# Optimization experiments

Hardware: AMD Instinct MI355X
Metric: run time of the kernel (lower is better)

## Reference

```python
import jax, jax.numpy as jnp
import numpy as np

HIDDEN = 1024
EMBED = HIDDEN // 4
SEQ = 512
BATCH = 256
NUM_CLASSES = 10


def setup_inputs() -> dict:
    key = jax.random.key(0)
    ks = jax.random.split(key, 16)

    def w(k, d1, d2):
        # kaiming_normal_ with nonlinearity='linear': std = 1/sqrt(fan_in=d2)
        return jax.random.normal(k, (d1, d2), dtype=jnp.float32) / jnp.sqrt(d2)

    inp = {
        "x": jax.random.randint(ks[0], (BATCH, SEQ), 0, 3),
        "emb": jax.random.normal(ks[1], (3, EMBED), dtype=jnp.float32),
        "w_gx": w(ks[2], EMBED, HIDDEN), "w_gh": w(ks[3], HIDDEN, HIDDEN), "b_g": jnp.zeros((HIDDEN,), jnp.float32),
        "w_ix": w(ks[4], EMBED, HIDDEN), "w_ih": w(ks[5], HIDDEN, HIDDEN), "b_i": jnp.zeros((HIDDEN,), jnp.float32),
        "w_fx": w(ks[6], EMBED, HIDDEN), "w_fh": w(ks[7], HIDDEN, HIDDEN), "b_f": jnp.zeros((HIDDEN,), jnp.float32),
        "w_ox": w(ks[8], EMBED, HIDDEN), "w_oh": w(ks[9], HIDDEN, HIDDEN), "b_o": jnp.zeros((HIDDEN,), jnp.float32),
        "w_ph": w(ks[10], HIDDEN, NUM_CLASSES), "b_p": jnp.zeros((NUM_CLASSES,), jnp.float32),
    }
    return inp


def reference(x, emb, w_gx, w_gh, b_g, w_ix, w_ih, b_i, w_fx, w_fh, b_f,
              w_ox, w_oh, b_o, w_ph, b_p):
    B, T = x.shape
    embedded = emb[x]                         # [B, T, E]
    pad = ((x + 1) // 2).astype(emb.dtype)    # [B, T]

    xs = (jnp.swapaxes(embedded, 0, 1),       # [T, B, E]
          jnp.swapaxes(pad, 0, 1))            # [T, B]

    h0 = jnp.zeros((B, w_gh.shape[0]), emb.dtype)
    c0 = jnp.zeros_like(h0)

    def step(carry, inputs):
        h, c = carry
        xt, pt = inputs
        g = jnp.tanh(xt @ w_gx + h @ w_gh + b_g)
        i = jax.nn.sigmoid(xt @ w_ix + h @ w_ih + b_i)
        f = jax.nn.sigmoid(xt @ w_fx + h @ w_fh + b_f)
        o = jax.nn.sigmoid(xt @ w_ox + h @ w_oh + b_o)
        c = g * i + c * f
        h = jnp.tanh(c) * o
        c = c * pt[:, None]
        return (h, c), None

    (h, _), _ = jax.lax.scan(step, (h0, c0), xs)
    p = h @ w_ph + b_p                        # [B, num_classes]
    # Faithful to original: log_softmax over dim=0 (batch dim)
    return jax.nn.log_softmax(p, axis=0)
```

## Files before the change

### kernel.cpp

```cpp
#include <hip/hip_runtime.h>
#include <hip/hip_bf16.h>

#define T_SEQ 512
#define BATCH 256
#define HID   1024
#define EMBD  256
#define NCLS  10

typedef __bf16 bf16x8 __attribute__((ext_vector_type(8)));
typedef float  floatx16 __attribute__((ext_vector_type(16)));
typedef float  floatx2 __attribute__((ext_vector_type(2)));
typedef unsigned short ushortx8 __attribute__((ext_vector_type(8)));

__device__ __forceinline__ unsigned int f2bf(float f) {
    unsigned int u = __builtin_bit_cast(unsigned int, f);
    u += 0x7fffu + ((u >> 16) & 1u);
    return u >> 16;
}
__device__ __forceinline__ float sig_fast(float x) {
    return __builtin_amdgcn_rcpf(1.0f + __expf(-x));
}
__device__ __forceinline__ float tanh_fast(float x) {
    return 1.0f - 2.0f * __builtin_amdgcn_rcpf(1.0f + __expf(2.0f * x));
}

__global__ void prep_xw_kernel(const float* __restrict__ emb,
                               const float* __restrict__ wgx, const float* __restrict__ wix,
                               const float* __restrict__ wfx, const float* __restrict__ wox,
                               const float* __restrict__ bg,  const float* __restrict__ bi,
                               const float* __restrict__ bf,  const float* __restrict__ bo,
                               float* __restrict__ XW) {
    int gid = blockIdx.x * blockDim.x + threadIdx.x;
    if (gid >= 3 * 4 * HID) return;
    int tok  = gid >> 12;
    int gate = (gid >> 10) & 3;
    int n    = gid & 1023;
    const float* W = gate == 0 ? wgx : gate == 1 ? wix : gate == 2 ? wfx : wox;
    const float* B = gate == 0 ? bg  : gate == 1 ? bi  : gate == 2 ? bf  : bo;
    float acc = B[n];
    const float* e = emb + tok * EMBD;
    for (int k = 0; k < EMBD; ++k) acc += e[k] * W[k * HID + n];
    XW[gid] = acc;
}

__global__ void prep_w_kernel(const float* __restrict__ wgh, const float* __restrict__ wih,
                              const float* __restrict__ wfh, const float* __restrict__ woh,
                              unsigned short* __restrict__ Wt) {
    int bid = blockIdx.x;
    int w   = bid & 31;
    int i   = (bid >> 5) & 31;
    int kh  = (bid >> 10) & 1;
    int g   = bid >> 11;
    const float* W = g == 0 ? wgh : g == 1 ? wih : g == 2 ? wfh : woh;
    int lane = threadIdx.x;
    int j    = w * 32 + (lane & 31);
    int k0   = kh * 512 + i * 16 + (lane >> 5) * 8;
    ushortx8 o8;
    #pragma unroll
    for (int e = 0; e < 8; ++e) o8[e] = (unsigned short)f2bf(W[(k0 + e) * HID + j]);
    int frag = ((w * 4 + g) * 2 + kh) * 32 + i;
    *(ushortx8*)&Wt[frag * 512 + lane * 8] = o8;
}

__global__ __launch_bounds__(512, 2)
void lstm_kernel(const int* __restrict__ x, const float* __restrict__ XW,
                 const unsigned short* __restrict__ Wt,
                 unsigned int* __restrict__ hbuf32, int* __restrict__ flags,
                 int* __restrict__ xflag) {
    __shared__ unsigned short hs[32 * 1032];
    __shared__ float gbuf[8 * 32 * 36];
    __shared__ float xwl[384];
    __shared__ unsigned char xtok[32 * 512];
    __shared__ int use_local_sh;

    const int tid  = threadIdx.x;
    const int grp  = blockIdx.x & 7;
    const int w    = blockIdx.x >> 3;
    const int wv   = tid >> 6;
    const int gv   = wv >> 1;
    const int kh   = wv & 1;
    const int lane = tid & 63;
    const int m32  = lane & 31;
    const int hv5  = lane >> 5;

    {
        int xcc = 0;
        asm volatile("s_getreg_b32 %0, hwreg(HW_REG_XCC_ID)" : "=s"(xcc));
        if (tid == 0) {
            __hip_atomic_store(&xflag[grp * 32 + w], xcc + 1, __ATOMIC_RELAXED,
                               __HIP_MEMORY_SCOPE_SYSTEM);
        }
        if (wv == 0) {
            int v;
            for (;;) {
                v = __hip_atomic_load(&xflag[grp * 32 + (lane & 31)], __ATOMIC_RELAXED,
                                      __HIP_MEMORY_SCOPE_SYSTEM);
                if (__all(v != 0)) break;
                __builtin_amdgcn_s_sleep(2);
            }
            int v0 = __shfl(v, 0, 64);
            if (lane == 0) use_local_sh = __all(v == v0) ? 1 : 0;
        }
    }

    bf16x8 Bf[32];
    {
        const unsigned short* wb = Wt + (size_t)(((w * 4 + gv) * 2 + kh) * 32) * 512
                                      + (size_t)lane * 8;
        #pragma unroll
        for (int i = 0; i < 32; ++i)
            Bf[i] = *(const bf16x8*)(wb + i * 512);
    }
    if (tid < 384) {
        int tok = tid >> 7, g = (tid >> 5) & 3, jl = tid & 31;
        xwl[tid] = XW[(tok * 4 + g) * HID + w * 32 + jl];
    }
    #pragma unroll
    for (int it = 0; it < 32; ++it) {
        int flat = it * 512 + tid;
        int row  = flat >> 9;
        int col  = flat & 511;
        xtok[flat] = (unsigned char)x[(grp * 32 + row) * T_SEQ + col];
    }
    __syncthreads();
    const bool use_local = (use_local_sh != 0);

    const int erow = tid >> 4;
    const int jc2  = tid & 15;
    float cst[2] = {0.f, 0.f};
    unsigned long long* hs64 = (unsigned long long*)hs;

    for (int s = 0; s < T_SEQ; ++s) {
        if (s > 0) {
            if (wv == 0) {
                const int fidx = grp * 32 + (lane & 31);
                if (use_local) {
                    while (__hip_atomic_load(&flags[fidx], __ATOMIC_RELAXED,
                                             __HIP_MEMORY_SCOPE_AGENT) < s)
                        __builtin_amdgcn_s_sleep(1);
                } else {
                    while (__hip_atomic_load(&flags[fidx], __ATOMIC_RELAXED,
                                             __HIP_MEMORY_SCOPE_SYSTEM) < s)
                        __builtin_amdgcn_s_sleep(1);
                }
            }
            __syncthreads();
        }

        const unsigned long long* hp64 = (const unsigned long long*)
            (hbuf32 + (size_t)(s & 1) * (BATCH * HID / 2)) + (size_t)grp * 32 * 256;
        {
            unsigned long long tmp[16];
            if (use_local) {
                #pragma unroll
                for (int it = 0; it < 16; ++it) {
                    int flat = it * 512 + tid;
                    tmp[it] = __hip_atomic_load(&hp64[(flat >> 8) * 256 + (flat & 255)],
                                                __ATOMIC_RELAXED, __HIP_MEMORY_SCOPE_AGENT);
                }
            } else {
                #pragma unroll
                for (int it = 0; it < 16; ++it) {
                    int flat = it * 512 + tid;
                    tmp[it] = __hip_atomic_load(&hp64[(flat >> 8) * 256 + (flat & 255)],
                                                __ATOMIC_RELAXED, __HIP_MEMORY_SCOPE_SYSTEM);
                }
            }
            #pragma unroll
            for (int it = 0; it < 16; ++it) {
                int flat = it * 512 + tid;
                hs64[(flat >> 8) * 258 + (flat & 255)] = tmp[it];
            }
        }
        __syncthreads();

        floatx16 acc = {0.f,0.f,0.f,0.f,0.f,0.f,0.f,0.f,0.f,0.f,0.f,0.f,0.f,0.f,0.f,0.f};
        const unsigned short* ap = hs + m32 * 1032 + kh * 512 + hv5 * 8;
        #pragma unroll
        for (int i = 0; i < 32; ++i) {
            bf16x8 a = *(const bf16x8*)(ap + i * 16);
            acc = __builtin_amdgcn_mfma_f32_32x32x16_bf16(a, Bf[i], acc, 0, 0, 0);
        }

        {
            float* gb = &gbuf[(size_t)(gv * 2 + kh) * 32 * 36];
            #pragma unroll
            for (int reg = 0; reg < 16; ++reg) {
                int row = (reg & 3) + 8 * (reg >> 2) + 4 * hv5;
                gb[row * 36 + m32] = acc[reg];
            }
        }
        __syncthreads();

        {
            int tk = xtok[erow * 512 + s];
            const float* xb = &xwl[tk * 128];
            const int go = erow * 36 + jc2 * 2;
            floatx2 ag = *(const floatx2*)&gbuf[0 * 32 * 36 + go]
                       + *(const floatx2*)&gbuf[1 * 32 * 36 + go];
            floatx2 ai = *(const floatx2*)&gbuf[2 * 32 * 36 + go]
                       + *(const floatx2*)&gbuf[3 * 32 * 36 + go];
            floatx2 af = *(const floatx2*)&gbuf[4 * 32 * 36 + go]
                       + *(const floatx2*)&gbuf[5 * 32 * 36 + go];
            floatx2 ao = *(const floatx2*)&gbuf[6 * 32 * 36 + go]
                       + *(const floatx2*)&gbuf[7 * 32 * 36 + go];
            floatx2 xg = *(const floatx2*)&xb[0 * 32 + jc2 * 2];
            floatx2 xi = *(const floatx2*)&xb[1 * 32 + jc2 * 2];
            floatx2 xf = *(const floatx2*)&xb[2 * 32 + jc2 * 2];
            floatx2 xo = *(const floatx2*)&xb[3 * 32 + jc2 * 2];
            unsigned int hvv[2];
            #pragma unroll
            for (int u = 0; u < 2; ++u) {
                float g  = tanh_fast(ag[u] + xg[u]);
                float ii = sig_fast(ai[u] + xi[u]);
                float ff = sig_fast(af[u] + xf[u]);
                float oo = sig_fast(ao[u] + xo[u]);
                float cn = g * ii + cst[u] * ff;
                float h  = tanh_fast(cn) * oo;
                cst[u]   = (tk != 0) ? cn : 0.0f;
                hvv[u]   = f2bf(h);
            }
            unsigned int* hnext = hbuf32 + (size_t)((s + 1) & 1) * (BATCH * HID / 2);
            unsigned int* hp = &hnext[((grp * 32 + erow) * HID + w * 32 + jc2 * 2) >> 1];
            unsigned int hval = hvv[0] | (hvv[1] << 16);
            if (use_local) {
                __hip_atomic_store(hp, hval, __ATOMIC_RELAXED, __HIP_MEMORY_SCOPE_WORKGROUP);
            } else {
                __hip_atomic_store(hp, hval, __ATOMIC_RELAXED, __HIP_MEMORY_SCOPE_SYSTEM);
            }
        }
        __syncthreads();

        if (s < T_SEQ - 1 && tid == 0) {
            if (use_local) {
                __hip_atomic_store(&flags[grp * 32 + w], s + 1,
                                   __ATOMIC_RELAXED, __HIP_MEMORY_SCOPE_WORKGROUP);
            } else {
                __hip_atomic_store(&flags[grp * 32 + w], s + 1,
                                   __ATOMIC_RELAXED, __HIP_MEMORY_SCOPE_SYSTEM);
            }
        }
    }
}

__global__ void proj_kernel(const unsigned short* __restrict__ h,
                            const float* __restrict__ wph, const float* __restrict__ bp,
                            float* __restrict__ out) {
    __shared__ float wl[HID * NCLS];
    __shared__ float red[256];
    int tid = threadIdx.x;
    for (int i = tid; i < HID * NCLS; i += 256) wl[i] = wph[i];
    __syncthreads();
    float p[NCLS];
    #pragma unroll
    for (int c2 = 0; c2 < NCLS; ++c2) p[c2] = bp[c2];
    const unsigned short* hr = h + tid * HID;
    for (int k0 = 0; k0 < HID / 8; ++k0) {
        bf16x8 hv = *(const bf16x8*)(hr + k0 * 8);
        #pragma unroll
        for (int j = 0; j < 8; ++j) {
            float hk = (float)hv[j];
            #pragma unroll
            for (int c2 = 0; c2 < NCLS; ++c2) p[c2] += hk * wl[(k0 * 8 + j) * NCLS + c2];
        }
    }
    for (int c2 = 0; c2 < NCLS; ++c2) {
        red[tid] = p[c2];
        __syncthreads();
        for (int s = 128; s > 0; s >>= 1) {
            if (tid < s) red[tid] = fmaxf(red[tid], red[tid + s]);
            __syncthreads();
        }
        float mx = red[0];
        __syncthreads();
        red[tid] = __expf(p[c2] - mx);
        __syncthreads();
        for (int s = 128; s > 0; s >>= 1) {
            if (tid < s) red[tid] += red[tid + s];
            __syncthreads();
        }
        float lse = mx + __logf(red[0]);
        __syncthreads();
        out[tid * NCLS + c2] = p[c2] - lse;
    }
}

extern "C" void kernel_launch(void* const* d_in, const int* in_sizes, int n_in,
                              void* d_out, int out_size, void* d_ws, size_t ws_size,
                              hipStream_t stream) {
    const int*   x    = (const int*)d_in[0];
    const float* emb  = (const float*)d_in[1];
    const float* wgx  = (const float*)d_in[2];
    const float* wgh  = (const float*)d_in[3];
    const float* bg_  = (const float*)d_in[4];
    const float* wix  = (const float*)d_in[5];
    const float* wih  = (const float*)d_in[6];
    const float* bi_  = (const float*)d_in[7];
    const float* wfx  = (const float*)d_in[8];
    const float* wfh  = (const float*)d_in[9];
    const float* bf_  = (const float*)d_in[10];
    const float* wox  = (const float*)d_in[11];
    const float* woh  = (const float*)d_in[12];
    const float* bo_  = (const float*)d_in[13];
    const float* wph  = (const float*)d_in[14];
    const float* bp_  = (const float*)d_in[15];
    float* out = (float*)d_out;

    char* wsp = (char*)d_ws;
    int*            flags = (int*)wsp;
    int*            xflag = (int*)(wsp + 4096);
    float*          XW    = (float*)(wsp + 8192);
    unsigned short* Wt    = (unsigned short*)(wsp + 8192 + 49152);
    unsigned int*   hbuf32= (unsigned int*)(wsp + 8192 + 49152 + 8388608);

    hipMemsetAsync(flags, 0, 8192, stream);
    hipMemsetAsync(hbuf32, 0, BATCH * HID * sizeof(unsigned short), stream);

    prep_xw_kernel<<<48, 256, 0, stream>>>(emb, wgx, wix, wfx, wox,
                                           bg_, bi_, bf_, bo_, XW);
    prep_w_kernel<<<8192, 64, 0, stream>>>(wgh, wih, wfh, woh, Wt);

    void* args[] = { (void*)&x, (void*)&XW, (void*)&Wt, (void*)&hbuf32,
                     (void*)&flags, (void*)&xflag };
    hipError_t cerr = hipLaunchCooperativeKernel((void*)lstm_kernel, dim3(256), dim3(512),
                                                 args, 0, stream);
    if (cerr != hipSuccess) {
        lstm_kernel<<<dim3(256), dim3(512), 0, stream>>>(x, XW, Wt, hbuf32, flags, xflag);
    }

    proj_kernel<<<1, 256, 0, stream>>>((const unsigned short*)hbuf32, wph, bp_, out);
}
```

Baseline: 1.777 ms.

## Read h directly from global into MFMA operands, split K four ways

```diff
diff --git a/kernel.cpp b/kernel.cpp
--- a/kernel.cpp
+++ b/kernel.cpp
@@ -46,19 +46,22 @@
 __global__ void prep_w_kernel(const float* __restrict__ wgh, const float* __restrict__ wih,
                               const float* __restrict__ wfh, const float* __restrict__ woh,
                               unsigned short* __restrict__ Wt) {
-    int bid = blockIdx.x;
-    int w   = bid & 31;
-    int i   = (bid >> 5) & 31;
-    int kh  = (bid >> 10) & 1;
-    int g   = bid >> 11;
+    int bid  = blockIdx.x;
+    int gsub = bid & 1;
+    int i    = (bid >> 1) & 15;
+    int kq   = (bid >> 5) & 3;
+    int gp   = (bid >> 7) & 1;
+    int w    = bid >> 8;
+    int g    = gp * 2 + gsub;
     const float* W = g == 0 ? wgh : g == 1 ? wih : g == 2 ? wfh : woh;
     int lane = threadIdx.x;
     int j    = w * 32 + (lane & 31);
-    int k0   = kh * 512 + i * 16 + (lane >> 5) * 8;
+    int kk   = kq * 16 + i;
+    int k0   = kk * 16 + (lane >> 5) * 8;
     ushortx8 o8;
     #pragma unroll
     for (int e = 0; e < 8; ++e) o8[e] = (unsigned short)f2bf(W[(k0 + e) * HID + j]);
-    int frag = ((w * 4 + g) * 2 + kh) * 32 + i;
+    int frag = (((w * 2 + gp) * 4 + kq) * 16 + i) * 2 + gsub;
     *(ushortx8*)&Wt[frag * 512 + lane * 8] = o8;
 }
 
@@ -67,8 +70,7 @@
                  const unsigned short* __restrict__ Wt,
                  unsigned int* __restrict__ hbuf32, int* __restrict__ flags,
                  int* __restrict__ xflag) {
-    __shared__ unsigned short hs[32 * 1032];
-    __shared__ float gbuf[8 * 32 * 36];
+    __shared__ float gbuf[16 * 32 * 36];
     __shared__ float xwl[384];
     __shared__ unsigned char xtok[32 * 512];
     __shared__ int use_local_sh;
@@ -77,8 +79,8 @@
     const int grp  = blockIdx.x & 7;
     const int w    = blockIdx.x >> 3;
     const int wv   = tid >> 6;
-    const int gv   = wv >> 1;
-    const int kh   = wv & 1;
+    const int gp   = wv >> 2;
+    const int kq   = wv & 3;
     const int lane = tid & 63;
     const int m32  = lane & 31;
     const int hv5  = lane >> 5;
@@ -105,11 +107,11 @@
 
     bf16x8 Bf[32];
     {
-        const unsigned short* wb = Wt + (size_t)(((w * 4 + gv) * 2 + kh) * 32) * 512
+        const unsigned short* wb = Wt + (size_t)(((w * 2 + gp) * 4 + kq) * 32) * 512
                                       + (size_t)lane * 8;
         #pragma unroll
-        for (int i = 0; i < 32; ++i)
-            Bf[i] = *(const bf16x8*)(wb + i * 512);
+        for (int t = 0; t < 32; ++t)
+            Bf[t] = *(const bf16x8*)(wb + t * 512);
     }
     if (tid < 384) {
         int tok = tid >> 7, g = (tid >> 5) & 3, jl = tid & 31;
@@ -128,7 +130,7 @@
     const int erow = tid >> 4;
     const int jc2  = tid & 15;
     float cst[2] = {0.f, 0.f};
-    unsigned long long* hs64 = (unsigned long long*)hs;
+    const unsigned short* hb = (const unsigned short*)hbuf32;
 
     for (int s = 0; s < T_SEQ; ++s) {
         if (s > 0) {
@@ -147,47 +149,38 @@
             __syncthreads();
         }
 
-        const unsigned long long* hp64 = (const unsigned long long*)
-            (hbuf32 + (size_t)(s & 1) * (BATCH * HID / 2)) + (size_t)grp * 32 * 256;
+        const unsigned short* hp = hb + (size_t)(s & 1) * (BATCH * HID)
+                                 + ((grp * 32 + m32) * HID + kq * 256 + hv5 * 8);
+        floatx16 acc0 = {0.f,0.f,0.f,0.f,0.f,0.f,0.f,0.f,0.f,0.f,0.f,0.f,0.f,0.f,0.f,0.f};
+        floatx16 acc1 = {0.f,0.f,0.f,0.f,0.f,0.f,0.f,0.f,0.f,0.f,0.f,0.f,0.f,0.f,0.f,0.f};
+        if (use_local) {
+            asm volatile("buffer_inv" ::: "memory");
+            #pragma unroll
+            for (int i = 0; i < 16; ++i) {
+                bf16x8 a = *(const bf16x8*)(hp + i * 16);
+                acc0 = __builtin_amdgcn_mfma_f32_32x32x16_bf16(a, Bf[2 * i],     acc0, 0, 0, 0);
+                acc1 = __builtin_amdgcn_mfma_f32_32x32x16_bf16(a, Bf[2 * i + 1], acc1, 0, 0, 0);
+            }
+        } else {
+            #pragma unroll
+            for (int i = 0; i < 16; ++i) {
+                union { unsigned long long q[2]; bf16x8 a; } u;
+                const unsigned long long* qp = (const unsigned long long*)(hp + i * 16);
+                u.q[0] = __hip_atomic_load(qp,     __ATOMIC_RELAXED, __HIP_MEMORY_SCOPE_SYSTEM);
+                u.q[1] = __hip_atomic_load(qp + 1, __ATOMIC_RELAXED, __HIP_MEMORY_SCOPE_SYSTEM);
+                acc0 = __builtin_amdgcn_mfma_f32_32x32x16_bf16(u.a, Bf[2 * i],     acc0, 0, 0, 0);
+                acc1 = __builtin_amdgcn_mfma_f32_32x32x16_bf16(u.a, Bf[2 * i + 1], acc1, 0, 0, 0);
+            }
+        }
+
         {
-            unsigned long long tmp[16];
-            if (use_local) {
-                #pragma unroll
-                for (int it = 0; it < 16; ++it) {
-                    int flat = it * 512 + tid;
-                    tmp[it] = __hip_atomic_load(&hp64[(flat >> 8) * 256 + (flat & 255)],
-                                                __ATOMIC_RELAXED, __HIP_MEMORY_SCOPE_AGENT);
-                }
-            } else {
-                #pragma unroll
-                for (int it = 0; it < 16; ++it) {
-                    int flat = it * 512 + tid;
-                    tmp[it] = __hip_atomic_load(&hp64[(flat >> 8) * 256 + (flat & 255)],
-                                                __ATOMIC_RELAXED, __HIP_MEMORY_SCOPE_SYSTEM);
-                }
-            }
-            #pragma unroll
-            for (int it = 0; it < 16; ++it) {
-                int flat = it * 512 + tid;
-                hs64[(flat >> 8) * 258 + (flat & 255)] = tmp[it];
-            }
-        }
-        __syncthreads();
-
-        floatx16 acc = {0.f,0.f,0.f,0.f,0.f,0.f,0.f,0.f,0.f,0.f,0.f,0.f,0.f,0.f,0.f,0.f};
-        const unsigned short* ap = hs + m32 * 1032 + kh * 512 + hv5 * 8;
-        #pragma unroll
-        for (int i = 0; i < 32; ++i) {
-            bf16x8 a = *(const bf16x8*)(ap + i * 16);
-            acc = __builtin_amdgcn_mfma_f32_32x32x16_bf16(a, Bf[i], acc, 0, 0, 0);
-        }
-
-        {
-            float* gb = &gbuf[(size_t)(gv * 2 + kh) * 32 * 36];
+            float* gb0 = &gbuf[(size_t)((gp * 2 + 0) * 4 + kq) * 1152];
+            float* gb1 = &gbuf[(size_t)((gp * 2 + 1) * 4 + kq) * 1152];
             #pragma unroll
             for (int reg = 0; reg < 16; ++reg) {
                 int row = (reg & 3) + 8 * (reg >> 2) + 4 * hv5;
-                gb[row * 36 + m32] = acc[reg];
+                gb0[row * 36 + m32] = acc0[reg];
+                gb1[row * 36 + m32] = acc1[reg];
             }
         }
         __syncthreads();
@@ -196,14 +189,15 @@
             int tk = xtok[erow * 512 + s];
             const float* xb = &xwl[tk * 128];
             const int go = erow * 36 + jc2 * 2;
-            floatx2 ag = *(const floatx2*)&gbuf[0 * 32 * 36 + go]
-                       + *(const floatx2*)&gbuf[1 * 32 * 36 + go];
-            floatx2 ai = *(const floatx2*)&gbuf[2 * 32 * 36 + go]
-                       + *(const floatx2*)&gbuf[3 * 32 * 36 + go];
-            floatx2 af = *(const floatx2*)&gbuf[4 * 32 * 36 + go]
-                       + *(const floatx2*)&gbuf[5 * 32 * 36 + go];
-            floatx2 ao = *(const floatx2*)&gbuf[6 * 32 * 36 + go]
-                       + *(const floatx2*)&gbuf[7 * 32 * 36 + go];
+            #define GSUM(g) ( *(const floatx2*)&gbuf[((g) * 4 + 0) * 1152 + go] \
+                            + *(const floatx2*)&gbuf[((g) * 4 + 1) * 1152 + go] \
+                            + *(const floatx2*)&gbuf[((g) * 4 + 2) * 1152 + go] \
+                            + *(const floatx2*)&gbuf[((g) * 4 + 3) * 1152 + go] )
+            floatx2 ag = GSUM(0);
+            floatx2 ai = GSUM(1);
+            floatx2 af = GSUM(2);
+            floatx2 ao = GSUM(3);
+            #undef GSUM
             floatx2 xg = *(const floatx2*)&xb[0 * 32 + jc2 * 2];
             floatx2 xi = *(const floatx2*)&xb[1 * 32 + jc2 * 2];
             floatx2 xf = *(const floatx2*)&xb[2 * 32 + jc2 * 2];
@@ -221,12 +215,12 @@
                 hvv[u]   = f2bf(h);
             }
             unsigned int* hnext = hbuf32 + (size_t)((s + 1) & 1) * (BATCH * HID / 2);
-            unsigned int* hp = &hnext[((grp * 32 + erow) * HID + w * 32 + jc2 * 2) >> 1];
+            unsigned int* hpst = &hnext[((grp * 32 + erow) * HID + w * 32 + jc2 * 2) >> 1];
             unsigned int hval = hvv[0] | (hvv[1] << 16);
             if (use_local) {
-                __hip_atomic_store(hp, hval, __ATOMIC_RELAXED, __HIP_MEMORY_SCOPE_WORKGROUP);
+                __hip_atomic_store(hpst, hval, __ATOMIC_RELAXED, __HIP_MEMORY_SCOPE_WORKGROUP);
             } else {
-                __hip_atomic_store(hp, hval, __ATOMIC_RELAXED, __HIP_MEMORY_SCOPE_SYSTEM);
+                __hip_atomic_store(hpst, hval, __ATOMIC_RELAXED, __HIP_MEMORY_SCOPE_SYSTEM);
             }
         }
         __syncthreads();
```

Result: slower. 2.643 ms (+48.7%).

## Split h-load into K halves with shared-memory counters instead of block barrier

Applied to the files above, without the earlier changes.

```diff
diff --git a/kernel.cpp b/kernel.cpp
--- a/kernel.cpp
+++ b/kernel.cpp
@@ -71,6 +71,7 @@
     __shared__ float gbuf[8 * 32 * 36];
     __shared__ float xwl[384];
     __shared__ unsigned char xtok[32 * 512];
+    __shared__ int scnt[2];
     __shared__ int use_local_sh;
 
     const int tid  = threadIdx.x;
@@ -115,6 +116,7 @@
         int tok = tid >> 7, g = (tid >> 5) & 3, jl = tid & 31;
         xwl[tid] = XW[(tok * 4 + g) * HID + w * 32 + jl];
     }
+    if (tid < 2) scnt[tid] = 0;
     #pragma unroll
     for (int it = 0; it < 32; ++it) {
         int flat = it * 512 + tid;
@@ -149,30 +151,74 @@
 
         const unsigned long long* hp64 = (const unsigned long long*)
             (hbuf32 + (size_t)(s & 1) * (BATCH * HID / 2)) + (size_t)grp * 32 * 256;
+
         {
+            unsigned long long tmp[8];
+            if (use_local) {
+                #pragma unroll
+                for (int it = 0; it < 8; ++it) {
+                    int flat = it * 512 + tid;
+                    tmp[it] = __hip_atomic_load(&hp64[(flat >> 7) * 256 + (flat & 127)],
+                                                __ATOMIC_RELAXED, __HIP_MEMORY_SCOPE_AGENT);
+                }
+            } else {
+                #pragma unroll
+                for (int it = 0; it < 8; ++it) {
+                    int flat = it * 512 + tid;
+                    tmp[it] = __hip_atomic_load(&hp64[(flat >> 7) * 256 + (flat & 127)],
+                                                __ATOMIC_RELAXED, __HIP_MEMORY_SCOPE_SYSTEM);
+                }
+            }
+            #pragma unroll
+            for (int it = 0; it < 8; ++it) {
+                int flat = it * 512 + tid;
+                hs64[(flat >> 7) * 258 + (flat & 127)] = tmp[it];
+            }
+            __builtin_amdgcn_fence(__ATOMIC_RELEASE, "workgroup");
+            if (lane == 0)
+                __hip_atomic_fetch_add(&scnt[0], 1, __ATOMIC_RELAXED,
+                                       __HIP_MEMORY_SCOPE_WORKGROUP);
+        }
+
+        if (kh == 0) {
+            const int t0 = 8 * (s + 1);
+            while (__hip_atomic_load(&scnt[0], __ATOMIC_RELAXED,
+                                     __HIP_MEMORY_SCOPE_WORKGROUP) < t0) {}
+            __builtin_amdgcn_fence(__ATOMIC_ACQUIRE, "workgroup");
+        } else {
             unsigned long long tmp[16];
+            const int p = ((wv >> 1) << 6) | lane;
             if (use_local) {
                 #pragma unroll
                 for (int it = 0; it < 16; ++it) {
-                    int flat = it * 512 + tid;
-                    tmp[it] = __hip_atomic_load(&hp64[(flat >> 8) * 256 + (flat & 255)],
-                                                __ATOMIC_RELAXED, __HIP_MEMORY_SCOPE_AGENT);
+                    int flat = it * 256 + p;
+                    tmp[it] = __hip_atomic_load(
+                        &hp64[(flat >> 7) * 256 + 128 + (flat & 127)],
+                        __ATOMIC_RELAXED, __HIP_MEMORY_SCOPE_AGENT);
                 }
             } else {
                 #pragma unroll
                 for (int it = 0; it < 16; ++it) {
-                    int flat = it * 512 + tid;
-                    tmp[it] = __hip_atomic_load(&hp64[(flat >> 8) * 256 + (flat & 255)],
-                                                __ATOMIC_RELAXED, __HIP_MEMORY_SCOPE_SYSTEM);
+                    int flat = it * 256 + p;
+                    tmp[it] = __hip_atomic_load(
+                        &hp64[(flat >> 7) * 256 + 128 + (flat & 127)],
+                        __ATOMIC_RELAXED, __HIP_MEMORY_SCOPE_SYSTEM);
                 }
             }
             #pragma unroll
             for (int it = 0; it < 16; ++it) {
-                int flat = it * 512 + tid;
-                hs64[(flat >> 8) * 258 + (flat & 255)] = tmp[it];
-            }
-        }
-        __syncthreads();
+                int flat = it * 256 + p;
+                hs64[(flat >> 7) * 258 + 128 + (flat & 127)] = tmp[it];
+            }
+            __builtin_amdgcn_fence(__ATOMIC_RELEASE, "workgroup");
+            if (lane == 0)
+                __hip_atomic_fetch_add(&scnt[1], 1, __ATOMIC_RELAXED,
+                                       __HIP_MEMORY_SCOPE_WORKGROUP);
+            const int t1 = 4 * (s + 1);
+            while (__hip_atomic_load(&scnt[1], __ATOMIC_RELAXED,
+                                     __HIP_MEMORY_SCOPE_WORKGROUP) < t1) {}
+            __builtin_amdgcn_fence(__ATOMIC_ACQUIRE, "workgroup");
+        }
 
         floatx16 acc = {0.f,0.f,0.f,0.f,0.f,0.f,0.f,0.f,0.f,0.f,0.f,0.f,0.f,0.f,0.f,0.f};
         const unsigned short* ap = hs + m32 * 1032 + kh * 512 + hv5 * 8;
```

Measured after the change: 1.799 ms. Within noise of the previous version (+1.2%).
